# Kernel optimization log

Hardware: AMD Instinct MI355X
Metric: run time of the kernel (lower is better)

The kernel has to match this reference:

```python
import jax, jax.numpy as jnp
import numpy as np
import math

B, N, NODE_DIM, EDGE_DIM, HID, NH = 2, 384, 128, 128, 128, 8
HD = HID // NH  # head_dim = 16


def _layernorm(x, g, b, eps=1e-5):
    m = jnp.mean(x, axis=-1, keepdims=True)
    v = jnp.var(x, axis=-1, keepdims=True)
    return (x - m) * jax.lax.rsqrt(v + eps) * g + b


def setup_inputs() -> dict:
    key = jax.random.key(0)
    ks = jax.random.split(key, 16)
    w = lambda k, s: jax.random.normal(k, s, jnp.float32) * 0.05
    return {
        "node_features": jax.random.normal(ks[0], (B, N, NODE_DIM), jnp.float32),
        "edge_features": jax.random.normal(ks[1], (B, N, N, EDGE_DIM), jnp.float32),
        "adj_mask": jax.random.randint(ks[2], (B, N, N), 0, 2, jnp.int32),
        "W_node": w(ks[3], (NODE_DIM, HID)), "b_node": jnp.zeros((HID,), jnp.float32),
        "W_q": w(ks[4], (HID, HID)), "b_q": jnp.zeros((HID,), jnp.float32),
        "W_k": w(ks[5], (HID, HID)), "b_k": jnp.zeros((HID,), jnp.float32),
        "W_v": w(ks[6], (HID, HID)), "b_v": jnp.zeros((HID,), jnp.float32),
        "W_edge": w(ks[7], (EDGE_DIM, HID)), "b_edge": jnp.zeros((HID,), jnp.float32),
        "W_gate": w(ks[8], (EDGE_DIM, HID)), "b_gate": jnp.zeros((HID,), jnp.float32),
        "W_out": w(ks[9], (HID, HID)), "b_out": jnp.zeros((HID,), jnp.float32),
        "W_eout": w(ks[10], (HID, EDGE_DIM)), "b_eout": jnp.zeros((EDGE_DIM,), jnp.float32),
        "g1": jnp.ones((HID,), jnp.float32), "be1": jnp.zeros((HID,), jnp.float32),
        "g2": jnp.ones((EDGE_DIM,), jnp.float32), "be2": jnp.zeros((EDGE_DIM,), jnp.float32),
    }


def reference(node_features, edge_features, adj_mask,
              W_node, b_node, W_q, b_q, W_k, b_k, W_v, b_v,
              W_edge, b_edge, W_gate, b_gate, W_out, b_out,
              W_eout, b_eout, g1, be1, g2, be2):
    b, n, _ = node_features.shape
    h = node_features @ W_node + b_node          # (B,N,HID)
    residual = h
    Q = (h @ W_q + b_q).reshape(b, n, NH, HD)
    K = (h @ W_k + b_k).reshape(b, n, NH, HD)
    V = (h @ W_v + b_v).reshape(b, n, NH, HD)
    scores = jnp.einsum('bihd,bjhd->bhij', Q, K) / math.sqrt(HD)  # (B,NH,N,N)
    # edge-gated bias
    edge_h = (edge_features @ W_edge + b_edge).reshape(b, n, n, NH, HD)
    edge_gate = jax.nn.sigmoid(edge_features @ W_gate + b_gate).reshape(b, n, n, NH, HD)
    edge_attn = jnp.sum(edge_h * edge_gate, axis=-1)  # (B,N,N,NH)
    scores = scores + jnp.transpose(edge_attn, (0, 3, 1, 2))
    # adjacency mask
    scores = jnp.where(adj_mask[:, None, :, :] == 0, jnp.float32(-1e9), scores)
    attn = jax.nn.softmax(scores, axis=-1)  # dropout = identity (eval)
    attn_out = jnp.einsum('bhij,bjhd->bihd', attn, V).reshape(b, n, HID)
    h = _layernorm(residual + (attn_out @ W_out + b_out), g1, be1)
    # edge update: mean attention over heads gates (src+tgt)/2
    attn_mean = jnp.mean(attn, axis=1)  # (B,N,N)
    pair = 0.5 * (h[:, :, None, :] + h[:, None, :, :])  # (B,N,N,HID)
    edge_update = attn_mean[..., None] * pair
    edge_out = _layernorm(edge_features + (edge_update @ W_eout + b_eout), g2, be2)
    return h, edge_out
```

## Files before the change

kernel.cpp:

```cpp
#include <hip/hip_runtime.h>
#include <hip/hip_bf16.h>

#define NN 384
#define HIDDIM 128
#define NHEADS 8
#define HD 16
#define LOCAL_E (NN*NN)
#define NE (2*LOCAL_E)
#define NNODE (2*NN)

typedef __attribute__((ext_vector_type(8))) __bf16 bf16x8;
typedef __attribute__((ext_vector_type(4))) float f32x4;

__global__ void prep_w(const float* __restrict__ W_edge, const float* __restrict__ W_gate,
                       bf16x8* __restrict__ Wg) {
    int gid = blockIdx.x * blockDim.x + threadIdx.x;
    int n16  = gid & 15;
    int quad = (gid >> 4) & 3;
    int kkl  = (gid >> 6) & 1;
    int np   = (gid >> 7) & 15;
    int kkh  = (gid >> 11) & 1;
    int n = np * 16 + n16;
    int k0 = (kkh * 2 + kkl) * 32 + quad * 8;
    const float* src = (n < 128) ? (W_edge + n) : (W_gate + (n - 128));
    bf16x8 v;
#pragma unroll
    for (int j = 0; j < 8; ++j) v[j] = (__bf16)src[(size_t)(k0 + j) * 128];
    Wg[gid] = v;
}

__global__ __launch_bounds__(128) void k1_proj(
    const float* __restrict__ nf,
    const float* __restrict__ Wn, const float* __restrict__ bn,
    const float* __restrict__ Wq, const float* __restrict__ bq,
    const float* __restrict__ Wk, const float* __restrict__ bk,
    const float* __restrict__ Wv, const float* __restrict__ bv,
    float* __restrict__ h_res, float* __restrict__ Q,
    float* __restrict__ K, float* __restrict__ V)
{
    __shared__ float xf[8][128];
    __shared__ float hf[8][128];
    int t = threadIdx.x;
    int r0 = blockIdx.x * 8;
    for (int r = 0; r < 8; ++r) xf[r][t] = nf[(size_t)(r0 + r) * 128 + t];
    __syncthreads();
    float acc[8];
#pragma unroll
    for (int r = 0; r < 8; ++r) acc[r] = bn[t];
    for (int k = 0; k < 128; ++k) {
        float w = Wn[k * 128 + t];
#pragma unroll
        for (int r = 0; r < 8; ++r) acc[r] += xf[r][k] * w;
    }
    for (int r = 0; r < 8; ++r) { h_res[(size_t)(r0 + r) * 128 + t] = acc[r]; hf[r][t] = acc[r]; }
    __syncthreads();
    const float* Ws[3] = {Wq, Wk, Wv};
    const float* bs[3] = {bq, bk, bv};
    float* Os[3] = {Q, K, V};
#pragma unroll
    for (int m = 0; m < 3; ++m) {
        float a2[8];
#pragma unroll
        for (int r = 0; r < 8; ++r) a2[r] = bs[m][t];
        for (int k = 0; k < 128; ++k) {
            float w = Ws[m][k * 128 + t];
#pragma unroll
            for (int r = 0; r < 8; ++r) a2[r] += hf[r][k] * w;
        }
        int hh = t >> 4, d = t & 15;
        for (int r = 0; r < 8; ++r) {
            int g = r0 + r;
            int b = g / NN, i = g - b * NN;
            Os[m][(size_t)((b * NHEADS + hh) * NN + i) * HD + d] = a2[r];
        }
    }
}

__global__ __launch_bounds__(512, 4) void k2_edge(
    const float* __restrict__ EF, const bf16x8* __restrict__ Wg,
    const float* __restrict__ b_edge, const float* __restrict__ b_gate,
    float* __restrict__ edge_attn)
{
    __shared__ bf16x8 Ash[2048];
    int t = threadIdx.x;
    int lane = t & 63;
    int w = t >> 6;
    int e_base = blockIdx.x * 128;

    bf16x8 wfh[4], wfg[4];
#pragma unroll
    for (int kk = 0; kk < 4; ++kk) {
        int kkh = kk >> 1, kkl = kk & 1;
        wfh[kk] = Wg[kkh * 2048 + ( w      * 2 + kkl) * 64 + lane];
        wfg[kk] = Wg[kkh * 2048 + ((w + 8) * 2 + kkl) * 64 + lane];
    }

#pragma unroll
    for (int p = 0; p < 4; ++p) {
        int gid = p * 512 + t;
        int m16 = gid & 15, quad = (gid >> 4) & 3, kk = (gid >> 6) & 3, ip = gid >> 8;
        int row = ip * 16 + m16;
        const float4* src4 = (const float4*)(EF + (size_t)(e_base + row) * 128
                                             + kk * 32 + quad * 8);
        float4 f0 = src4[0], f1 = src4[1];
        bf16x8 v;
        v[0] = (__bf16)f0.x; v[1] = (__bf16)f0.y; v[2] = (__bf16)f0.z; v[3] = (__bf16)f0.w;
        v[4] = (__bf16)f1.x; v[5] = (__bf16)f1.y; v[6] = (__bf16)f1.z; v[7] = (__bf16)f1.w;
        Ash[gid] = v;
    }
    __syncthreads();

    f32x4 acc_h[8], acc_g[8];
    f32x4 zero = {0.f, 0.f, 0.f, 0.f};
#pragma unroll
    for (int ip = 0; ip < 8; ++ip) { acc_h[ip] = zero; acc_g[ip] = zero; }

#pragma unroll
    for (int kk = 0; kk < 4; ++kk) {
#pragma unroll
        for (int ip = 0; ip < 8; ++ip) {
            bf16x8 be = Ash[(ip * 4 + kk) * 64 + lane];
            acc_h[ip] = __builtin_amdgcn_mfma_f32_16x16x32_bf16(wfh[kk], be, acc_h[ip], 0, 0, 0);
            acc_g[ip] = __builtin_amdgcn_mfma_f32_16x16x32_bf16(wfg[kk], be, acc_g[ip], 0, 0, 0);
        }
    }

    int n16 = lane & 15, quad = lane >> 4;
    float bh[4], bg[4];
#pragma unroll
    for (int r = 0; r < 4; ++r) {
        bh[r] = b_edge[w * 16 + quad * 4 + r];
        bg[r] = b_gate[w * 16 + quad * 4 + r];
    }
#pragma unroll
    for (int ip = 0; ip < 8; ++ip) {
        float s = 0.f;
#pragma unroll
        for (int r = 0; r < 4; ++r) {
            float hv = acc_h[ip][r] + bh[r];
            float gv = acc_g[ip][r] + bg[r];
            float sig = __builtin_amdgcn_rcpf(1.f + __expf(-gv));
            s = fmaf(hv, sig, s);
        }
        s += __shfl_xor(s, 16);
        s += __shfl_xor(s, 32);
        if (quad == 0) {
            int e = e_base + ip * 16 + n16;
            int b = e / LOCAL_E;
            int local = e - b * LOCAL_E;
            edge_attn[(size_t)(b * NHEADS + w) * LOCAL_E + local] = s;
        }
    }
}

__global__ __launch_bounds__(128) void k3_attn(
    const float* __restrict__ Q, const float* __restrict__ K, const float* __restrict__ V,
    const float* __restrict__ edge_attn, const int* __restrict__ adj,
    float* __restrict__ am, float* __restrict__ attn_out)
{
    __shared__ float Kh[NN * 17];
    __shared__ float Vh[NN * 17];
    __shared__ float Qi[16 * HD];
    __shared__ float rowbuf[NN];
    __shared__ float red[2];
    __shared__ float red2[8][16];
    int t = threadIdx.x;
    int bh = blockIdx.x / 24;
    int chunk = blockIdx.x % 24;
    int b = bh >> 3;
    const float* Kbase = K + (size_t)bh * NN * HD;
    const float* Vbase = V + (size_t)bh * NN * HD;
    for (int p = 0; p < 48; ++p) {
        int idx = p * 128 + t;
        int jj = idx >> 4, dd = idx & 15;
        Kh[jj * 17 + dd] = Kbase[idx];
        Vh[jj * 17 + dd] = Vbase[idx];
    }
    Qi[t]       = Q[(size_t)bh * NN * HD + chunk * 16 * HD + t];
    Qi[t + 128] = Q[(size_t)bh * NN * HD + chunk * 16 * HD + t + 128];
    __syncthreads();
    int lane = t & 63, wid = t >> 6;
    const float* ea = edge_attn + (size_t)bh * LOCAL_E;
    const int* adjb = adj + (size_t)b * LOCAL_E;
    for (int rr = 0; rr < 16; ++rr) {
        int i = chunk * 16 + rr;
        float s[3];
#pragma unroll
        for (int jj = 0; jj < 3; ++jj) {
            int j = t + jj * 128;
            float a = 0.f;
#pragma unroll
            for (int d = 0; d < 16; ++d) a += Qi[rr * 16 + d] * Kh[j * 17 + d];
            a = a * 0.25f + ea[(size_t)i * NN + j];
            if (adjb[(size_t)i * NN + j] == 0) a = -1e9f;
            s[jj] = a;
        }
        float mx = fmaxf(s[0], fmaxf(s[1], s[2]));
#pragma unroll
        for (int o = 1; o < 64; o <<= 1) mx = fmaxf(mx, __shfl_xor(mx, o));
        if (lane == 0) red[wid] = mx;
        __syncthreads();
        mx = fmaxf(red[0], red[1]);
        __syncthreads();
        float e0 = __expf(s[0] - mx), e1 = __expf(s[1] - mx), e2 = __expf(s[2] - mx);
        float sm = e0 + e1 + e2;
#pragma unroll
        for (int o = 1; o < 64; o <<= 1) sm += __shfl_xor(sm, o);
        if (lane == 0) red[wid] = sm;
        __syncthreads();
        float inv = 1.f / (red[0] + red[1]);
        float p0 = e0 * inv, p1 = e1 * inv, p2 = e2 * inv;
        rowbuf[t] = p0; rowbuf[t + 128] = p1; rowbuf[t + 256] = p2;
        atomicAdd(am + (size_t)b * LOCAL_E + i * NN + t,       p0 * 0.125f);
        atomicAdd(am + (size_t)b * LOCAL_E + i * NN + t + 128, p1 * 0.125f);
        atomicAdd(am + (size_t)b * LOCAL_E + i * NN + t + 256, p2 * 0.125f);
        __syncthreads();
        int d = t & 15, g = t >> 4;
        float pa = 0.f;
        for (int j = g * 48; j < g * 48 + 48; ++j) pa += rowbuf[j] * Vh[j * 17 + d];
        red2[g][d] = pa;
        __syncthreads();
        if (t < 16) {
            float s2 = 0.f;
#pragma unroll
            for (int gg = 0; gg < 8; ++gg) s2 += red2[gg][t];
            attn_out[(size_t)(b * NN + i) * HIDDIM + (bh & 7) * HD + t] = s2;
        }
        __syncthreads();
    }
}

__global__ __launch_bounds__(128) void k5_hout(
    const float* __restrict__ attn_out, const float* __restrict__ h_res,
    const float* __restrict__ W_out, const float* __restrict__ b_out,
    const float* __restrict__ g1, const float* __restrict__ be1,
    const float* __restrict__ W_eout,
    float* __restrict__ h_out, float* __restrict__ hp)
{
    __shared__ float ao[8][128];
    __shared__ float hn[8][128];
    __shared__ float redA[2], redB[2];
    int t = threadIdx.x, r0 = blockIdx.x * 8;
    for (int r = 0; r < 8; ++r) ao[r][t] = attn_out[(size_t)(r0 + r) * 128 + t];
    __syncthreads();
    float acc[8];
#pragma unroll
    for (int r = 0; r < 8; ++r) acc[r] = b_out[t];
    for (int k = 0; k < 128; ++k) {
        float w = W_out[k * 128 + t];
#pragma unroll
        for (int r = 0; r < 8; ++r) acc[r] += ao[r][k] * w;
    }
    int lane = t & 63, wid = t >> 6;
    float gg = g1[t], bb = be1[t];
    for (int r = 0; r < 8; ++r) {
        float u = h_res[(size_t)(r0 + r) * 128 + t] + acc[r];
        float sv = u, sq = u * u;
#pragma unroll
        for (int o = 1; o < 64; o <<= 1) { sv += __shfl_xor(sv, o); sq += __shfl_xor(sq, o); }
        if (lane == 0) { redA[wid] = sv; redB[wid] = sq; }
        __syncthreads();
        float tot = redA[0] + redA[1], totq = redB[0] + redB[1];
        __syncthreads();
        float mean = tot * (1.f / 128.f);
        float var = totq * (1.f / 128.f) - mean * mean;
        float nv = (u - mean) * rsqrtf(var + 1e-5f) * gg + bb;
        h_out[(size_t)(r0 + r) * 128 + t] = nv;
        hn[r][t] = nv;
    }
    __syncthreads();
    float acc2[8];
#pragma unroll
    for (int r = 0; r < 8; ++r) acc2[r] = 0.f;
    for (int k = 0; k < 128; ++k) {
        float w = W_eout[k * 128 + t];
#pragma unroll
        for (int r = 0; r < 8; ++r) acc2[r] += hn[r][k] * w;
    }
    for (int r = 0; r < 8; ++r) hp[(size_t)(r0 + r) * 128 + t] = acc2[r];
}

__global__ __launch_bounds__(256) void k6_eout(
    const float* __restrict__ EF, const float* __restrict__ am,
    const float* __restrict__ hp, const float* __restrict__ b_eout,
    const float* __restrict__ g2, const float* __restrict__ be2,
    float* __restrict__ eout)
{
    int t = threadIdx.x;
    int slot = t >> 5, l = t & 31;
    int e = blockIdx.x * 8 + slot;
    int b = e / LOCAL_E;
    int local = e - b * LOCAL_E;
    int i = local / NN, j = local - i * NN;
    float a = am[e];
    const float4* ef4 = (const float4*)(EF + (size_t)e * 128);
    const float4* hpi = (const float4*)(hp + (size_t)(b * NN + i) * 128);
    const float4* hpj = (const float4*)(hp + (size_t)(b * NN + j) * 128);
    float4 ef = ef4[l];
    float4 pi = hpi[l], pj = hpj[l];
    float4 bo = ((const float4*)b_eout)[l];
    float4 u;
    u.x = ef.x + a * 0.5f * (pi.x + pj.x) + bo.x;
    u.y = ef.y + a * 0.5f * (pi.y + pj.y) + bo.y;
    u.z = ef.z + a * 0.5f * (pi.z + pj.z) + bo.z;
    u.w = ef.w + a * 0.5f * (pi.w + pj.w) + bo.w;
    float sv = u.x + u.y + u.z + u.w;
    float sq = u.x * u.x + u.y * u.y + u.z * u.z + u.w * u.w;
#pragma unroll
    for (int o = 1; o < 32; o <<= 1) { sv += __shfl_xor(sv, o); sq += __shfl_xor(sq, o); }
    float mean = sv * (1.f / 128.f);
    float var = sq * (1.f / 128.f) - mean * mean;
    float rs = rsqrtf(var + 1e-5f);
    float4 gg = ((const float4*)g2)[l], bb = ((const float4*)be2)[l];
    float4 o4;
    o4.x = (u.x - mean) * rs * gg.x + bb.x;
    o4.y = (u.y - mean) * rs * gg.y + bb.y;
    o4.z = (u.z - mean) * rs * gg.z + bb.z;
    o4.w = (u.w - mean) * rs * gg.w + bb.w;
    ((float4*)(eout + (size_t)e * 128))[l] = o4;
}

extern "C" void kernel_launch(void* const* d_in, const int* in_sizes, int n_in,
                              void* d_out, int out_size, void* d_ws, size_t ws_size,
                              hipStream_t stream) {
    (void)in_sizes; (void)n_in; (void)out_size; (void)ws_size;
    const float* nf     = (const float*)d_in[0];
    const float* ef     = (const float*)d_in[1];
    const int*   adj    = (const int*)d_in[2];
    const float* W_node = (const float*)d_in[3];
    const float* b_node = (const float*)d_in[4];
    const float* W_q    = (const float*)d_in[5];
    const float* b_q    = (const float*)d_in[6];
    const float* W_k    = (const float*)d_in[7];
    const float* b_k    = (const float*)d_in[8];
    const float* W_v    = (const float*)d_in[9];
    const float* b_v    = (const float*)d_in[10];
    const float* W_edge = (const float*)d_in[11];
    const float* b_edge = (const float*)d_in[12];
    const float* W_gate = (const float*)d_in[13];
    const float* b_gate = (const float*)d_in[14];
    const float* W_out  = (const float*)d_in[15];
    const float* b_out  = (const float*)d_in[16];
    const float* W_eout = (const float*)d_in[17];
    const float* b_eout = (const float*)d_in[18];
    const float* g1     = (const float*)d_in[19];
    const float* be1    = (const float*)d_in[20];
    const float* g2     = (const float*)d_in[21];
    const float* be2    = (const float*)d_in[22];

    float* ws = (float*)d_ws;
    float* h_res    = ws;
    float* Q        = ws + 98304;
    float* Kp       = ws + 196608;
    float* Vp       = ws + 294912;
    float* attn_out = ws + 393216;
    float* hp       = ws + 491520;
    float* am       = ws + 589824;
    bf16x8* Wg      = (bf16x8*)(ws + 884736);

    float* h_out = (float*)d_out;
    float* eout  = (float*)d_out + 98304;
    float* edge_attn = eout;

    prep_w<<<dim3(16), dim3(256), 0, stream>>>(W_edge, W_gate, Wg);
    k1_proj<<<dim3(96), dim3(128), 0, stream>>>(nf, W_node, b_node, W_q, b_q,
                                                W_k, b_k, W_v, b_v, h_res, Q, Kp, Vp);
    k2_edge<<<dim3(2304), dim3(512), 0, stream>>>(ef, Wg, b_edge, b_gate, edge_attn);
    hipMemsetAsync((void*)am, 0, (size_t)NE * sizeof(float), stream);
    k3_attn<<<dim3(384), dim3(128), 0, stream>>>(Q, Kp, Vp, edge_attn, adj, am, attn_out);
    k5_hout<<<dim3(96), dim3(128), 0, stream>>>(attn_out, h_res, W_out, b_out,
                                                g1, be1, W_eout, h_out, hp);
    k6_eout<<<dim3(36864), dim3(256), 0, stream>>>(ef, am, hp, b_eout, g2, be2, eout);
}
```

Measured before the change: 451.0 us.

## Restructure attention kernel to one wave per query row with no block barriers

```diff
diff --git a/kernel.cpp b/kernel.cpp
--- a/kernel.cpp
+++ b/kernel.cpp
@@ -153,80 +153,88 @@
     }
 }
 
-__global__ __launch_bounds__(128) void k3_attn(
+__global__ __launch_bounds__(256) void k3_attn(
     const float* __restrict__ Q, const float* __restrict__ K, const float* __restrict__ V,
     const float* __restrict__ edge_attn, const int* __restrict__ adj,
     float* __restrict__ am, float* __restrict__ attn_out)
 {
     __shared__ float Kh[NN * 17];
-    __shared__ float Vh[NN * 17];
+    __shared__ float Vh[NN * 16];
     __shared__ float Qi[16 * HD];
-    __shared__ float rowbuf[NN];
-    __shared__ float red[2];
-    __shared__ float red2[8][16];
+    __shared__ float rowbuf[4][NN];
     int t = threadIdx.x;
+    int lane = t & 63, wid = t >> 6;
     int bh = blockIdx.x / 24;
     int chunk = blockIdx.x % 24;
-    int b = bh >> 3;
-    const float* Kbase = K + (size_t)bh * NN * HD;
-    const float* Vbase = V + (size_t)bh * NN * HD;
-    for (int p = 0; p < 48; ++p) {
-        int idx = p * 128 + t;
-        int jj = idx >> 4, dd = idx & 15;
-        Kh[jj * 17 + dd] = Kbase[idx];
-        Vh[jj * 17 + dd] = Vbase[idx];
-    }
-    Qi[t]       = Q[(size_t)bh * NN * HD + chunk * 16 * HD + t];
-    Qi[t + 128] = Q[(size_t)bh * NN * HD + chunk * 16 * HD + t + 128];
-    __syncthreads();
-    int lane = t & 63, wid = t >> 6;
+    int b = bh >> 3, h = bh & 7;
+    const float4* K4 = (const float4*)(K + (size_t)bh * NN * HD);
+    const float4* V4 = (const float4*)(V + (size_t)bh * NN * HD);
+#pragma unroll
+    for (int p = 0; p < 6; ++p) {
+        int idx4 = p * 256 + t;
+        int j = idx4 >> 2, d0 = (idx4 & 3) * 4;
+        float4 kv = K4[idx4];
+        Kh[j * 17 + d0]     = kv.x;
+        Kh[j * 17 + d0 + 1] = kv.y;
+        Kh[j * 17 + d0 + 2] = kv.z;
+        Kh[j * 17 + d0 + 3] = kv.w;
+        ((float4*)Vh)[idx4] = V4[idx4];
+    }
+    Qi[t] = Q[(size_t)bh * NN * HD + chunk * 16 * HD + t];
+    __syncthreads();
+
     const float* ea = edge_attn + (size_t)bh * LOCAL_E;
     const int* adjb = adj + (size_t)b * LOCAL_E;
-    for (int rr = 0; rr < 16; ++rr) {
+    float* amb = am + (size_t)b * LOCAL_E;
+    int jg = lane >> 4, d = lane & 15;
+
+    for (int r = 0; r < 4; ++r) {
+        int rr = wid * 4 + r;
         int i = chunk * 16 + rr;
-        float s[3];
-#pragma unroll
-        for (int jj = 0; jj < 3; ++jj) {
-            int j = t + jj * 128;
+        float ql[16];
+#pragma unroll
+        for (int dd = 0; dd < 16; ++dd) ql[dd] = Qi[rr * 16 + dd];
+        const float* ea_row = ea + (size_t)i * NN;
+        const int* adj_row = adjb + (size_t)i * NN;
+        float s[6];
+#pragma unroll
+        for (int jj = 0; jj < 6; ++jj) {
+            int j = jj * 64 + lane;
             float a = 0.f;
 #pragma unroll
-            for (int d = 0; d < 16; ++d) a += Qi[rr * 16 + d] * Kh[j * 17 + d];
-            a = a * 0.25f + ea[(size_t)i * NN + j];
-            if (adjb[(size_t)i * NN + j] == 0) a = -1e9f;
+            for (int dd = 0; dd < 16; ++dd) a = fmaf(ql[dd], Kh[j * 17 + dd], a);
+            a = a * 0.25f + ea_row[j];
+            if (adj_row[j] == 0) a = -1e9f;
             s[jj] = a;
         }
-        float mx = fmaxf(s[0], fmaxf(s[1], s[2]));
+        float mx = s[0];
+#pragma unroll
+        for (int jj = 1; jj < 6; ++jj) mx = fmaxf(mx, s[jj]);
 #pragma unroll
         for (int o = 1; o < 64; o <<= 1) mx = fmaxf(mx, __shfl_xor(mx, o));
-        if (lane == 0) red[wid] = mx;
-        __syncthreads();
-        mx = fmaxf(red[0], red[1]);
-        __syncthreads();
-        float e0 = __expf(s[0] - mx), e1 = __expf(s[1] - mx), e2 = __expf(s[2] - mx);
-        float sm = e0 + e1 + e2;
+        float sm = 0.f;
+#pragma unroll
+        for (int jj = 0; jj < 6; ++jj) { s[jj] = __expf(s[jj] - mx); sm += s[jj]; }
 #pragma unroll
         for (int o = 1; o < 64; o <<= 1) sm += __shfl_xor(sm, o);
-        if (lane == 0) red[wid] = sm;
-        __syncthreads();
-        float inv = 1.f / (red[0] + red[1]);
-        float p0 = e0 * inv, p1 = e1 * inv, p2 = e2 * inv;
-        rowbuf[t] = p0; rowbuf[t + 128] = p1; rowbuf[t + 256] = p2;
-        atomicAdd(am + (size_t)b * LOCAL_E + i * NN + t,       p0 * 0.125f);
-        atomicAdd(am + (size_t)b * LOCAL_E + i * NN + t + 128, p1 * 0.125f);
-        atomicAdd(am + (size_t)b * LOCAL_E + i * NN + t + 256, p2 * 0.125f);
-        __syncthreads();
-        int d = t & 15, g = t >> 4;
+        float inv = 1.f / sm;
+#pragma unroll
+        for (int jj = 0; jj < 6; ++jj) {
+            int j = jj * 64 + lane;
+            float p = s[jj] * inv;
+            rowbuf[wid][j] = p;
+            atomicAdd(amb + (size_t)i * NN + j, p * 0.125f);
+        }
         float pa = 0.f;
-        for (int j = g * 48; j < g * 48 + 48; ++j) pa += rowbuf[j] * Vh[j * 17 + d];
-        red2[g][d] = pa;
-        __syncthreads();
-        if (t < 16) {
-            float s2 = 0.f;
-#pragma unroll
-            for (int gg = 0; gg < 8; ++gg) s2 += red2[gg][t];
-            attn_out[(size_t)(b * NN + i) * HIDDIM + (bh & 7) * HD + t] = s2;
-        }
-        __syncthreads();
+#pragma unroll 4
+        for (int ss = 0; ss < 96; ++ss) {
+            int j = ss * 4 + jg;
+            pa = fmaf(rowbuf[wid][j], Vh[j * 16 + d], pa);
+        }
+        pa += __shfl_xor(pa, 16);
+        pa += __shfl_xor(pa, 32);
+        if (lane < 16)
+            attn_out[(size_t)(b * NN + i) * HIDDIM + h * HD + lane] = pa;
     }
 }
 
@@ -367,7 +375,7 @@
                                                 W_k, b_k, W_v, b_v, h_res, Q, Kp, Vp);
     k2_edge<<<dim3(2304), dim3(512), 0, stream>>>(ef, Wg, b_edge, b_gate, edge_attn);
     hipMemsetAsync((void*)am, 0, (size_t)NE * sizeof(float), stream);
-    k3_attn<<<dim3(384), dim3(128), 0, stream>>>(Q, Kp, Vp, edge_attn, adj, am, attn_out);
+    k3_attn<<<dim3(384), dim3(256), 0, stream>>>(Q, Kp, Vp, edge_attn, adj, am, attn_out);
     k5_hout<<<dim3(96), dim3(128), 0, stream>>>(attn_out, h_res, W_out, b_out,
                                                 g1, be1, W_eout, h_out, hp);
     k6_eout<<<dim3(36864), dim3(256), 0, stream>>>(ef, am, hp, b_eout, g2, be2, eout);
```

New measurement: 437.8 us. -2.9%, faster.
